# Kernel optimization log

Hardware: AMD Instinct MI355X
Metric: run time of the kernel (lower is better)

The kernel has to match this reference:

```python
import math
import jax, jax.numpy as jnp
import numpy as np

B, N, D, Pd, L, H = 2, 384, 256, 64, 8, 8
Dh = D // H
VOCAB = 21


def _layernorm(x, w, b, eps=1e-5):
    m = jnp.mean(x, axis=-1, keepdims=True)
    v = jnp.var(x, axis=-1, keepdims=True)
    return (x - m) * jax.lax.rsqrt(v + eps) * w + b


def _safe_norm(v):
    return jnp.sqrt(jnp.sum(v * v, axis=-1, keepdims=True) + 1e-8)


def _rot6d(r6):
    # Zhou et al. 6D rotation -> 3x3 via Gram-Schmidt (rows b1,b2,b3)
    a1, a2 = r6[..., :3], r6[..., 3:6]
    b1 = a1 / _safe_norm(a1)
    a2p = a2 - jnp.sum(b1 * a2, axis=-1, keepdims=True) * b1
    b2 = a2p / _safe_norm(a2p)
    b3 = jnp.cross(b1, b2)
    return jnp.stack([b1, b2, b3], axis=-2)  # [..., 3, 3]


def _pos_enc(n, d):
    pos = jnp.arange(n, dtype=jnp.float32)[:, None]
    div = jnp.exp(jnp.arange(0, d, 2, dtype=jnp.float32) * (-math.log(10000.0) / d))
    ang = pos * div  # [n, d/2]
    return jnp.zeros((n, d), jnp.float32).at[:, 0::2].set(jnp.sin(ang)).at[:, 1::2].set(jnp.cos(ang))


def _se3_frame_attention(Q, K, V, frames):
    # Frame-conditioned attention: dot-product scores biased by squared
    # distance between frame translations (IPA-style point bias).
    t = frames[..., :3, 3]                                   # [B,N,3]
    d2 = jnp.sum((t[:, :, None] - t[:, None, :]) ** 2, -1)   # [B,N,N]
    s = jnp.einsum('bihd,bjhd->bhij', Q, K) / math.sqrt(Dh) - d2[:, None]
    a = jax.nn.softmax(s, axis=-1)
    return jnp.einsum('bhij,bjhd->bihd', a, V)               # [B,N,H,Dh]


def _encode(tokens, tok_emb, emb_ln_w, emb_ln_b, Wq, Wk, Wv, Wo, bo,
            attn_ln_w, attn_ln_b, ff_ln_w, ff_ln_b, W1, b1, W2, b2,
            Wop, bop, relpos_emb, pair_ln_w, pair_ln_b, Wf1, bf1, Wf2, bf2):
    Bb, Nn = tokens.shape
    x = tok_emb[tokens] + _pos_enc(Nn, D)[None]
    x = _layernorm(x, emb_ln_w, emb_ln_b)
    frames = jnp.broadcast_to(jnp.eye(4, dtype=x.dtype), (Bb, Nn, 4, 4))
    pos = jnp.arange(Nn)
    rel = jnp.clip(pos[None, :] - pos[:, None], -64, 64) + 64  # rel[i,j]=pos[j]-pos[i]
    rel_e = relpos_emb[rel]                                    # [N,N,Pd]
    bot = jnp.broadcast_to(jnp.array([0.0, 0.0, 0.0, 1.0], x.dtype), (Bb, Nn, 1, 4))
    for l in range(L):
        # SE3 attention block (dropout = identity in eval)
        Q = (x @ Wq[l]).reshape(Bb, Nn, H, Dh)
        Kh = (x @ Wk[l]).reshape(Bb, Nn, H, Dh)
        Vh = (x @ Wv[l]).reshape(Bb, Nn, H, Dh)
        ao = _se3_frame_attention(Q, Kh, Vh, frames).reshape(Bb, Nn, D)
        x = _layernorm(x + ao @ Wo[l] + bo[l], attn_ln_w[l], attn_ln_b[l])
        # FFN (pre-LN inside the Sequential), residual add
        h = _layernorm(x, ff_ln_w[l], ff_ln_b[l])
        x = x + (jax.nn.gelu(h @ W1[l] + b1[l], approximate=False) @ W2[l] + b2[l])
        # Pair features
        proj = jax.nn.relu(x @ Wop + bop)                      # [B,N,Pd]
        pair = _layernorm(proj[:, :, None] + proj[:, None, :] + rel_e[None],
                          pair_ln_w, pair_ln_b)                # [B,N,N,Pd]
        # Frame head
        feat = jnp.concatenate([x, pair.mean(axis=2)], axis=-1)
        raw = jax.nn.silu(feat @ Wf1 + bf1) @ Wf2 + bf2        # [B,N,9]
        R = _rot6d(raw[..., :6])
        trans = raw[..., 6:]
        top = jnp.concatenate([R, trans[..., None]], axis=-1)  # [B,N,3,4]
        frames = jnp.concatenate([top, bot], axis=-2)          # [B,N,4,4]
    return frames, x


def setup_inputs() -> dict:
    key = jax.random.key(0)
    ks = iter(jax.random.split(key, 16))
    def w(shape, scale):
        return (jax.random.normal(next(ks), shape) * scale).astype(jnp.float32)
    return {
        'tokens': jax.random.randint(next(ks), (B, N), 0, VOCAB, dtype=jnp.int32),
        'tok_emb': w((VOCAB, D), 0.02),
        'emb_ln_w': jnp.ones((D,), jnp.float32), 'emb_ln_b': jnp.zeros((D,), jnp.float32),
        'Wq': w((L, D, D), D ** -0.5), 'Wk': w((L, D, D), D ** -0.5),
        'Wv': w((L, D, D), D ** -0.5), 'Wo': w((L, D, D), D ** -0.5),
        'bo': jnp.zeros((L, D), jnp.float32),
        'attn_ln_w': jnp.ones((L, D), jnp.float32), 'attn_ln_b': jnp.zeros((L, D), jnp.float32),
        'ff_ln_w': jnp.ones((L, D), jnp.float32), 'ff_ln_b': jnp.zeros((L, D), jnp.float32),
        'W1': w((L, D, 4 * D), D ** -0.5), 'b1': jnp.zeros((L, 4 * D), jnp.float32),
        'W2': w((L, 4 * D, D), (4 * D) ** -0.5), 'b2': jnp.zeros((L, D), jnp.float32),
        'Wop': w((D, Pd), D ** -0.5), 'bop': jnp.zeros((Pd,), jnp.float32),
        'relpos_emb': w((129, Pd), 0.02),
        'pair_ln_w': jnp.ones((Pd,), jnp.float32), 'pair_ln_b': jnp.zeros((Pd,), jnp.float32),
        'Wf1': w((D + Pd, 128), (D + Pd) ** -0.5), 'bf1': jnp.zeros((128,), jnp.float32),
        'Wf2': w((128, 9), 128 ** -0.5), 'bf2': jnp.zeros((9,), jnp.float32),
    }


def reference(tokens, tok_emb, emb_ln_w, emb_ln_b, Wq, Wk, Wv, Wo, bo,
              attn_ln_w, attn_ln_b, ff_ln_w, ff_ln_b, W1, b1, W2, b2,
              Wop, bop, relpos_emb, pair_ln_w, pair_ln_b, Wf1, bf1, Wf2, bf2):
    return _encode(tokens, tok_emb, emb_ln_w, emb_ln_b, Wq, Wk, Wv, Wo, bo,
                   attn_ln_w, attn_ln_b, ff_ln_w, ff_ln_b, W1, b1, W2, b2,
                   Wop, bop, relpos_emb, pair_ln_w, pair_ln_b, Wf1, bf1, Wf2, bf2)
```

## Files before the change

### kernel.cpp

```cpp
#include <hip/hip_runtime.h>
#include <hip/hip_bf16.h>
#include <math.h>

#define B_  2
#define N_  384
#define D_  256
#define PD_ 64
#define L_  8
#define H_  8
#define DH_ 32
#define GR  4
#define IT  8
#define RT_ 132

__global__ void prologue_kernel(const int* __restrict__ tokens, const float* __restrict__ tok_emb,
                                const float* __restrict__ lnw, const float* __restrict__ lnb,
                                const float* __restrict__ relpos,
                                float* __restrict__ x, float* __restrict__ frames,
                                float* __restrict__ tx, float* __restrict__ ty,
                                float* __restrict__ tz,
                                float* __restrict__ relc, float* __restrict__ relcT) {
  int row = blockIdx.x;
  int n = row % N_;
  int d = threadIdx.x;
  __shared__ float rbuf[256];
  __shared__ float smr;
  if (d < 16) frames[row * 16 + d] = (d == 0 || d == 5 || d == 10 || d == 15) ? 1.0f : 0.0f;
  if (d == 16) tx[row] = 0.0f;
  if (d == 17) ty[row] = 0.0f;
  if (d == 18) tz[row] = 0.0f;
  if (row < 129 && d >= 192) {
    int lane = d & 63;
    float s = relpos[row * PD_ + lane];
    #pragma unroll
    for (int off = 32; off >= 1; off >>= 1) s += __shfl_xor(s, off, 64);
    if (lane == 0) smr = s * (1.0f / PD_);
  }
  int tok = tokens[row];
  float val = tok_emb[tok * D_ + d];
  int i = d >> 1;
  float dv = expf((float)(2 * i) * (-logf(10000.0f) / (float)D_));
  float ang = (float)n * dv;
  val += (d & 1) ? cosf(ang) : sinf(ang);
  rbuf[d] = val; __syncthreads();
  for (int s = 128; s > 0; s >>= 1) { if (d < s) rbuf[d] += rbuf[d + s]; __syncthreads(); }
  float mean = rbuf[0] / D_;
  __syncthreads();
  rbuf[d] = val * val; __syncthreads();
  for (int s = 128; s > 0; s >>= 1) { if (d < s) rbuf[d] += rbuf[d + s]; __syncthreads(); }
  float var = rbuf[0] / D_ - mean * mean;
  float r = rsqrtf(var + 1e-5f);
  x[row * D_ + d] = (val - mean) * r * lnw[d] + lnb[d];
  if (row < 129 && d < PD_) {
    float cv = relpos[row * PD_ + d] - smr;
    relc[row * PD_ + d] = cv;
    relcT[d * RT_ + row] = cv;
  }
}

__device__ __forceinline__ void qkv_unit(int bid, int tid, const float* __restrict__ x,
                                         const float* __restrict__ Wq, const float* __restrict__ Wk,
                                         const float* __restrict__ Wv,
                                         float* __restrict__ q, float* __restrict__ kt,
                                         float* __restrict__ v, float* sA) {
  int tile = bid & 3;
  int m = (bid >> 2) % 3;
  int r0 = (bid / 12) * GR;
  float* red = sA + GR * D_;
  {
    int r = tid >> 6, lane = tid & 63;
    ((float4*)(sA + r * D_))[lane] = ((const float4*)(x + (size_t)(r0 + r) * D_))[lane];
  }
  __syncthreads();
  const float* W = (m == 0) ? Wq : (m == 1) ? Wk : Wv;
  int kc = tid >> 6, c = tid & 63;
  const float* wp = W + (size_t)(kc * 64) * D_ + tile * 64 + c;
  const float* s0 = sA + kc * 64;
  float a0 = 0.f, a1 = 0.f, a2 = 0.f, a3 = 0.f;
  for (int kk = 0; kk < 64; kk += 4) {
    float w0 = wp[(size_t)kk * D_], w1 = wp[(size_t)(kk + 1) * D_];
    float w2 = wp[(size_t)(kk + 2) * D_], w3 = wp[(size_t)(kk + 3) * D_];
    float4 h0 = *(const float4*)(s0 + 0 * D_ + kk);
    float4 h1 = *(const float4*)(s0 + 1 * D_ + kk);
    float4 h2 = *(const float4*)(s0 + 2 * D_ + kk);
    float4 h3 = *(const float4*)(s0 + 3 * D_ + kk);
    a0 = fmaf(h0.x, w0, fmaf(h0.y, w1, fmaf(h0.z, w2, fmaf(h0.w, w3, a0))));
    a1 = fmaf(h1.x, w0, fmaf(h1.y, w1, fmaf(h1.z, w2, fmaf(h1.w, w3, a1))));
    a2 = fmaf(h2.x, w0, fmaf(h2.y, w1, fmaf(h2.z, w2, fmaf(h2.w, w3, a2))));
    a3 = fmaf(h3.x, w0, fmaf(h3.y, w1, fmaf(h3.z, w2, fmaf(h3.w, w3, a3))));
  }
  red[(kc * 4 + 0) * 64 + c] = a0;
  red[(kc * 4 + 1) * 64 + c] = a1;
  red[(kc * 4 + 2) * 64 + c] = a2;
  red[(kc * 4 + 3) * 64 + c] = a3;
  __syncthreads();
  int r = tid >> 6;
  float s = red[(0 * 4 + r) * 64 + c] + red[(1 * 4 + r) * 64 + c]
          + red[(2 * 4 + r) * 64 + c] + red[(3 * 4 + r) * 64 + c];
  int col = tile * 64 + c;
  int row = r0 + r;
  if (m == 1) {
    int b = row / N_, j = row % N_;
    int hh = col >> 5, dd = col & 31;
    kt[((size_t)(b * H_ + hh) * DH_ + dd) * N_ + j] = s;
  } else {
    float* O = (m == 0) ? q : v;
    O[(size_t)row * D_ + col] = s;
  }
}

__device__ __forceinline__ void proj_unit(int row, int tid, const float* __restrict__ x,
                                          const float* __restrict__ Wop, const float* __restrict__ bop,
                                          float* __restrict__ projc, float* __restrict__ projcT,
                                          float* smem) {
  float* sA  = smem;
  float* red = smem + 256;
  if (tid < 64) ((float4*)sA)[tid] = ((const float4*)(x + (size_t)row * D_))[tid];
  __syncthreads();
  int kc = tid >> 6, c = tid & 63;
  const float* wp = Wop + (kc * 64) * PD_ + c;
  const float* s0 = sA + kc * 64;
  float a0 = 0.f, a1 = 0.f, a2 = 0.f, a3 = 0.f;
  for (int kk = 0; kk < 64; kk += 4) {
    a0 = fmaf(s0[kk],     wp[(kk)     * PD_], a0);
    a1 = fmaf(s0[kk + 1], wp[(kk + 1) * PD_], a1);
    a2 = fmaf(s0[kk + 2], wp[(kk + 2) * PD_], a2);
    a3 = fmaf(s0[kk + 3], wp[(kk + 3) * PD_], a3);
  }
  red[kc * 64 + c] = (a0 + a1) + (a2 + a3);
  __syncthreads();
  if (tid < 64) {
    float acc = fmaxf(bop[tid] + red[tid] + red[64 + tid] + red[128 + tid] + red[192 + tid], 0.0f);
    float s = acc;
    #pragma unroll
    for (int off = 32; off >= 1; off >>= 1) s += __shfl_xor(s, off, 64);
    float cv = acc - s * (1.0f / PD_);
    projc[row * PD_ + tid] = cv;
    projcT[(size_t)tid * (B_ * N_) + row] = cv;
  }
}

__global__ void qkv_kernel(const float* __restrict__ x, const float* __restrict__ Wq,
                           const float* __restrict__ Wk, const float* __restrict__ Wv,
                           float* __restrict__ q, float* __restrict__ kt, float* __restrict__ v) {
  __shared__ __align__(16) float smem[2048];
  qkv_unit(blockIdx.x, threadIdx.x, x, Wq, Wk, Wv, q, kt, v, smem);
}

__global__ void proj_qkv_kernel(const float* __restrict__ x,
                                const float* __restrict__ Wop, const float* __restrict__ bop,
                                float* __restrict__ projc, float* __restrict__ projcT,
                                const float* __restrict__ Wq, const float* __restrict__ Wk,
                                const float* __restrict__ Wv,
                                float* __restrict__ q, float* __restrict__ kt,
                                float* __restrict__ v) {
  __shared__ __align__(16) float smem[2048];
  int bid = blockIdx.x, tid = threadIdx.x;
  if (bid < B_ * N_) proj_unit(bid, tid, x, Wop, bop, projc, projcT, smem);
  else               qkv_unit(bid - B_ * N_, tid, x, Wq, Wk, Wv, q, kt, v, smem);
}

__global__ void wo_ln_kernel(const float* __restrict__ ao, const float* __restrict__ Wo,
                             const float* __restrict__ bo,
                             const float* __restrict__ lnw, const float* __restrict__ lnb,
                             float* __restrict__ x) {
  int r0 = blockIdx.x * 2;
  int tid = threadIdx.x;
  int wave = tid >> 6, lane = tid & 63;
  __shared__ __align__(16) float sAO[2 * D_];
  __shared__ float wred[4][4];
  if (tid < 128) ((float4*)sAO)[tid] = ((const float4*)(ao + (size_t)r0 * D_))[tid];
  __syncthreads();
  const float* wp = Wo + tid;
  float a0 = 0.f, a1 = 0.f, a2 = 0.f, a3 = 0.f;
  float c0 = 0.f, c1 = 0.f, c2 = 0.f, c3 = 0.f;
  for (int kk = 0; kk < D_; kk += 4) {
    float w0 = wp[(size_t)kk * D_], w1 = wp[(size_t)(kk + 1) * D_];
    float w2 = wp[(size_t)(kk + 2) * D_], w3 = wp[(size_t)(kk + 3) * D_];
    float4 h0 = *(const float4*)(sAO + kk);
    float4 h1 = *(const float4*)(sAO + D_ + kk);
    a0 = fmaf(h0.x, w0, a0); a1 = fmaf(h0.y, w1, a1);
    a2 = fmaf(h0.z, w2, a2); a3 = fmaf(h0.w, w3, a3);
    c0 = fmaf(h1.x, w0, c0); c1 = fmaf(h1.y, w1, c1);
    c2 = fmaf(h1.z, w2, c2); c3 = fmaf(h1.w, w3, c3);
  }
  float bb = bo[tid];
  float v0 = x[(size_t)r0 * D_ + tid]       + bb + (a0 + a1) + (a2 + a3);
  float v1 = x[(size_t)(r0 + 1) * D_ + tid] + bb + (c0 + c1) + (c2 + c3);
  float s0 = v0, q0 = v0 * v0, s1 = v1, q1 = v1 * v1;
  #pragma unroll
  for (int off = 32; off >= 1; off >>= 1) {
    s0 += __shfl_xor(s0, off, 64); q0 += __shfl_xor(q0, off, 64);
    s1 += __shfl_xor(s1, off, 64); q1 += __shfl_xor(q1, off, 64);
  }
  if (lane == 0) {
    wred[0][wave] = s0; wred[1][wave] = q0;
    wred[2][wave] = s1; wred[3][wave] = q1;
  }
  __syncthreads();
  float S0 = wred[0][0] + wred[0][1] + wred[0][2] + wred[0][3];
  float Q0 = wred[1][0] + wred[1][1] + wred[1][2] + wred[1][3];
  float S1 = wred[2][0] + wred[2][1] + wred[2][2] + wred[2][3];
  float Q1 = wred[3][0] + wred[3][1] + wred[3][2] + wred[3][3];
  float m0 = S0 * (1.0f / D_), m1 = S1 * (1.0f / D_);
  float r0v = rsqrtf(Q0 * (1.0f / D_) - m0 * m0 + 1e-5f);
  float r1v = rsqrtf(Q1 * (1.0f / D_) - m1 * m1 + 1e-5f);
  float wv = lnw[tid], bv = lnb[tid];
  x[(size_t)r0 * D_ + tid]       = (v0 - m0) * r0v * wv + bv;
  x[(size_t)(r0 + 1) * D_ + tid] = (v1 - m1) * r1v * wv + bv;
}

__global__ void gemm4t_kernel(const float* __restrict__ A, const float* __restrict__ W,
                              const float* __restrict__ bias, const float* __restrict__ resid,
                              float* __restrict__ C, int K, int Nc) {
  int tiles = Nc >> 5;
  int bid = blockIdx.x;
  int tile = bid % tiles;
  int r0 = (bid / tiles) * GR;
  int tid = threadIdx.x;
  extern __shared__ __align__(16) float sA[];
  float* red = sA + GR * K;
  {
    int r = tid >> 6, lane = tid & 63;
    for (int kk = lane; kk < (K >> 2); kk += 64)
      ((float4*)(sA + r * K))[kk] = ((const float4*)(A + (size_t)(r0 + r) * K))[kk];
  }
  __syncthreads();
  int kc = tid >> 5, c = tid & 31;
  int KC = K >> 3;
  const float* wp = W + (size_t)(kc * KC) * Nc + tile * 32 + c;
  const float* s0 = sA + kc * KC;
  float a0 = 0.f, a1 = 0.f, a2 = 0.f, a3 = 0.f;
  for (int kk = 0; kk < KC; kk += 4) {
    float w0 = wp[(size_t)kk * Nc], w1 = wp[(size_t)(kk + 1) * Nc];
    float w2 = wp[(size_t)(kk + 2) * Nc], w3 = wp[(size_t)(kk + 3) * Nc];
    float4 h0 = *(const float4*)(s0 + 0 * K + kk);
    float4 h1 = *(const float4*)(s0 + 1 * K + kk);
    float4 h2 = *(const float4*)(s0 + 2 * K + kk);
    float4 h3 = *(const float4*)(s0 + 3 * K + kk);
    a0 = fmaf(h0.x, w0, fmaf(h0.y, w1, fmaf(h0.z, w2, fmaf(h0.w, w3, a0))));
    a1 = fmaf(h1.x, w0, fmaf(h1.y, w1, fmaf(h1.z, w2, fmaf(h1.w, w3, a1))));
    a2 = fmaf(h2.x, w0, fmaf(h2.y, w1, fmaf(h2.z, w2, fmaf(h2.w, w3, a2))));
    a3 = fmaf(h3.x, w0, fmaf(h3.y, w1, fmaf(h3.z, w2, fmaf(h3.w, w3, a3))));
  }
  red[(kc * 4 + 0) * 32 + c] = a0;
  red[(kc * 4 + 1) * 32 + c] = a1;
  red[(kc * 4 + 2) * 32 + c] = a2;
  red[(kc * 4 + 3) * 32 + c] = a3;
  __syncthreads();
  if (tid < GR * 32) {
    int r = tid >> 5, cc = tid & 31;
    float s = 0.f;
    #pragma unroll
    for (int k8 = 0; k8 < 8; k8++) s += red[(k8 * 4 + r) * 32 + cc];
    int col = tile * 32 + cc;
    if (bias)  s += bias[col];
    if (resid) s += resid[(size_t)(r0 + r) * Nc + col];
    C[(size_t)(r0 + r) * Nc + col] = s;
  }
}

__global__ void ff1_kernel(const float* __restrict__ x,
                           const float* __restrict__ lnw, const float* __restrict__ lnb,
                           const float* __restrict__ W1, const float* __restrict__ b1,
                           float* __restrict__ f) {
  int bid = blockIdx.x;
  int tile = bid & 7;
  int r0 = (bid >> 3) * GR;
  int tid = threadIdx.x;
  __shared__ __align__(16) float sA[GR * D_];
  __shared__ float red[2 * GR * 128];
  {
    int r = tid >> 6, lane = tid & 63;
    float4 v = ((const float4*)(x + (size_t)(r0 + r) * D_))[lane];
    float s = v.x + v.y + v.z + v.w;
    float s2 = v.x * v.x + v.y * v.y + v.z * v.z + v.w * v.w;
    #pragma unroll
    for (int off = 32; off >= 1; off >>= 1) {
      s  += __shfl_xor(s, off, 64);
      s2 += __shfl_xor(s2, off, 64);
    }
    float mean = s * (1.0f / D_);
    float var = s2 * (1.0f / D_) - mean * mean;
    float rin = rsqrtf(var + 1e-5f);
    float4 w4 = ((const float4*)lnw)[lane];
    float4 b4 = ((const float4*)lnb)[lane];
    float4 nv;
    nv.x = (v.x - mean) * rin * w4.x + b4.x;
    nv.y = (v.y - mean) * rin * w4.y + b4.y;
    nv.z = (v.z - mean) * rin * w4.z + b4.z;
    nv.w = (v.w - mean) * rin * w4.w + b4.w;
    ((float4*)(sA + r * D_))[lane] = nv;
  }
  __syncthreads();
  int kc = tid >> 7, c = tid & 127;
  int col = tile * 128 + c;
  const float* wp = W1 + (size_t)(kc * 128) * 1024 + col;
  const float* s0 = sA + kc * 128;
  float a0 = 0.f, a1 = 0.f, a2 = 0.f, a3 = 0.f;
  for (int kk = 0; kk < 128; kk += 4) {
    float w0 = wp[(size_t)kk * 1024], w1 = wp[(size_t)(kk + 1) * 1024];
    float w2 = wp[(size_t)(kk + 2) * 1024], w3 = wp[(size_t)(kk + 3) * 1024];
    float4 h0 = *(const float4*)(s0 + 0 * D_ + kk);
    float4 h1 = *(const float4*)(s0 + 1 * D_ + kk);
    float4 h2 = *(const float4*)(s0 + 2 * D_ + kk);
    float4 h3 = *(const float4*)(s0 + 3 * D_ + kk);
    a0 = fmaf(h0.x, w0, fmaf(h0.y, w1, fmaf(h0.z, w2, fmaf(h0.w, w3, a0))));
    a1 = fmaf(h1.x, w0, fmaf(h1.y, w1, fmaf(h1.z, w2, fmaf(h1.w, w3, a1))));
    a2 = fmaf(h2.x, w0, fmaf(h2.y, w1, fmaf(h2.z, w2, fmaf(h2.w, w3, a2))));
    a3 = fmaf(h3.x, w0, fmaf(h3.y, w1, fmaf(h3.z, w2, fmaf(h3.w, w3, a3))));
  }
  red[(kc * 4 + 0) * 128 + c] = a0;
  red[(kc * 4 + 1) * 128 + c] = a1;
  red[(kc * 4 + 2) * 128 + c] = a2;
  red[(kc * 4 + 3) * 128 + c] = a3;
  __syncthreads();
  int rA = tid >> 7;
  #pragma unroll
  for (int p = 0; p < 2; p++) {
    int r = rA + p * 2;
    float s = red[(0 * 4 + r) * 128 + c] + red[(1 * 4 + r) * 128 + c] + b1[col];
    s = 0.5f * s * (1.0f + erff(s * 0.7071067811865475f));
    f[(size_t)(r0 + r) * 1024 + col] = s;
  }
}

__global__ void attn_kernel(const float* __restrict__ Q, const float* __restrict__ KT,
                            const float* __restrict__ V,
                            const float* __restrict__ tx, const float* __restrict__ ty,
                            const float* __restrict__ tz, float* __restrict__ AO) {
  const int TILES = N_ / IT;
  int bid = blockIdx.x;
  int it = bid % TILES;
  int h  = (bid / TILES) % H_;
  int b  = bid / (TILES * H_);
  int i0 = it * IT;
  int tid = threadIdx.x;
  int wave = tid >> 6, lane = tid & 63;

  __shared__ __align__(16) float sQ[IT * DH_];
  __shared__ __align__(16) float sK[DH_ * 64];
  __shared__ __align__(16) float sV[64 * DH_];
  __shared__ __align__(16) float sS[IT][N_];
  __shared__ float sti[3][IT];
  __shared__ float sinv[IT];

  {
    int ii = tid >> 5, d = tid & 31;
    sQ[ii * DH_ + d] = Q[((size_t)(b * N_ + i0 + ii)) * D_ + h * DH_ + d];
  }
  if (tid < IT) {
    sti[0][tid] = tx[b * N_ + i0 + tid];
    sti[1][tid] = ty[b * N_ + i0 + tid];
    sti[2][tid] = tz[b * N_ + i0 + tid];
  }
  const float* ktb = KT + (size_t)(b * H_ + h) * DH_ * N_;
  const float* vb  = V + (size_t)b * N_ * D_ + h * DH_;
  const float* txb = tx + b * N_;
  const float* tyb = ty + b * N_;
  const float* tzb = tz + b * N_;
  __syncthreads();

  float4 q0r[8], q1r[8];
  #pragma unroll
  for (int t = 0; t < 8; t++) {
    q0r[t] = ((const float4*)(sQ + (wave * 2 + 0) * DH_))[t];
    q1r[t] = ((const float4*)(sQ + (wave * 2 + 1) * DH_))[t];
  }

  for (int jc = 0; jc < N_; jc += 64) {
    for (int idx = tid; idx < DH_ * 64; idx += 256) {
      int d = idx >> 6, jj = idx & 63;
      sK[d * 64 + jj] = ktb[(size_t)d * N_ + jc + jj];
    }
    __syncthreads();
    int jj = lane;
    float tjx = txb[jc + jj], tjy = tyb[jc + jj], tjz = tzb[jc + jj];
    float a0 = 0.f, a1 = 0.f;
    #pragma unroll
    for (int t = 0; t < 8; t++) {
      float k0 = sK[(4 * t + 0) * 64 + jj];
      float k1 = sK[(4 * t + 1) * 64 + jj];
      float k2 = sK[(4 * t + 2) * 64 + jj];
      float k3 = sK[(4 * t + 3) * 64 + jj];
      float4 qa = q0r[t], qb = q1r[t];
      a0 = fmaf(qa.x, k0, fmaf(qa.y, k1, fmaf(qa.z, k2, fmaf(qa.w, k3, a0))));
      a1 = fmaf(qb.x, k0, fmaf(qb.y, k1, fmaf(qb.z, k2, fmaf(qb.w, k3, a1))));
    }
    #pragma unroll
    for (int s = 0; s < 2; s++) {
      int ii = wave * 2 + s;
      float a = (s == 0) ? a0 : a1;
      float dx = sti[0][ii] - tjx;
      float dy = sti[1][ii] - tjy;
      float dz = sti[2][ii] - tjz;
      sS[ii][jc + jj] = a * 0.17677669529663689f - (dx * dx + dy * dy + dz * dz);
    }
    __syncthreads();
  }

  #pragma unroll
  for (int s = 0; s < 2; s++) {
    int ii = wave * 2 + s;
    float vrow[6];
    float m = -1e30f;
    #pragma unroll
    for (int t = 0; t < 6; t++) { vrow[t] = sS[ii][t * 64 + lane]; m = fmaxf(m, vrow[t]); }
    #pragma unroll
    for (int off = 32; off >= 1; off >>= 1) m = fmaxf(m, __shfl_xor(m, off, 64));
    float ps = 0.f;
    #pragma unroll
    for (int t = 0; t < 6; t++) {
      float e = expf(vrow[t] - m);
      sS[ii][t * 64 + lane] = e;
      ps += e;
    }
    #pragma unroll
    for (int off = 32; off >= 1; off >>= 1) ps += __shfl_xor(ps, off, 64);
    if (lane == 0) sinv[ii] = 1.0f / ps;
  }
  __syncthreads();

  int ii = tid >> 5, dd = tid & 31;
  float o0 = 0.f, o1 = 0.f;
  for (int jc = 0; jc < N_; jc += 64) {
    for (int idx = tid; idx < 64 * DH_; idx += 256) {
      int jj = idx >> 5, d = idx & 31;
      sV[jj * DH_ + d] = vb[(size_t)(jc + jj) * D_ + d];
    }
    __syncthreads();
    const float* srow = &sS[ii][jc];
    #pragma unroll
    for (int jj = 0; jj < 64; jj += 4) {
      float4 sv = *(const float4*)(srow + jj);
      o0 = fmaf(sv.x, sV[(jj + 0) * DH_ + dd], o0);
      o1 = fmaf(sv.y, sV[(jj + 1) * DH_ + dd], o1);
      o0 = fmaf(sv.z, sV[(jj + 2) * DH_ + dd], o0);
      o1 = fmaf(sv.w, sV[(jj + 3) * DH_ + dd], o1);
    }
    __syncthreads();
  }
  AO[((size_t)(b * N_ + i0 + ii)) * D_ + h * DH_ + dd] = (o0 + o1) * sinv[ii];
}

__global__ void pair_head_kernel(const float* __restrict__ projc, const float* __restrict__ projcT,
                                 const float* __restrict__ relc, const float* __restrict__ relcT,
                                 const float* __restrict__ lnw, const float* __restrict__ lnb,
                                 const float* __restrict__ x,
                                 const float* __restrict__ Wf1, const float* __restrict__ bWf1,
                                 const float* __restrict__ Wf2, const float* __restrict__ bWf2,
                                 float* __restrict__ frames, float* __restrict__ tx,
                                 float* __restrict__ ty, float* __restrict__ tz) {
  const int M = B_ * N_;
  int row = blockIdx.x;
  int b = row / N_;
  int i = row % N_;
  int tid = threadIdx.x;
  int lane = tid & 63;
  int wave = tid >> 6;
  __shared__ float svpi[PD_];
  __shared__ float sr[N_];
  __shared__ float red[4][PD_];
  __shared__ float sfeat[320];
  __shared__ float fred[2][128];
  __shared__ float sg[128];
  __shared__ float sraw[9];

  if (tid < PD_) svpi[tid] = projc[row * PD_ + tid];
  if (tid < D_) sfeat[tid] = x[(size_t)row * D_ + tid];
  __syncthreads();

  {
    int jA = tid;
    int raA = jA - i; raA = raA < -64 ? -64 : (raA > 64 ? 64 : raA); raA += 64;
    const float* pA = projcT + b * N_ + jA;
    const float* rA = relcT + raA;
    float s2A = 0.f;
    #pragma unroll 8
    for (int c = 0; c < PD_; c++) {
      float dA = svpi[c] + pA[(size_t)c * M] + rA[c * RT_];
      s2A = fmaf(dA, dA, s2A);
    }
    sr[jA] = rsqrtf(s2A * (1.0f / PD_) + 1e-5f);
    if (tid < 128) {
      int jB = tid + 256;
      int raB = jB - i; raB = raB < -64 ? -64 : (raB > 64 ? 64 : raB); raB += 64;
      const float* pB = projcT + b * N_ + jB;
      const float* rB = relcT + raB;
      float s2B = 0.f;
      #pragma unroll 8
      for (int c = 0; c < PD_; c++) {
        float dB = svpi[c] + pB[(size_t)c * M] + rB[c * RT_];
        s2B = fmaf(dB, dB, s2B);
      }
      sr[jB] = rsqrtf(s2B * (1.0f / PD_) + 1e-5f);
    }
  }
  __syncthreads();

  {
    float vpl = svpi[lane];
    const float* pb = projc + (size_t)b * N_ * PD_;
    float acc = 0.0f;
    for (int j = wave * 2; j < N_; j += 8) {
      int ja = j, jb = j + 1;
      int ra = ja - i; ra = ra < -64 ? -64 : (ra > 64 ? 64 : ra); ra += 64;
      int rb = jb - i; rb = rb < -64 ? -64 : (rb > 64 ? 64 : rb); rb += 64;
      float da = vpl + pb[ja * PD_ + lane] + relc[ra * PD_ + lane];
      float db = vpl + pb[jb * PD_ + lane] + relc[rb * PD_ + lane];
      acc = fmaf(da, sr[ja], fmaf(db, sr[jb], acc));
    }
    red[wave][lane] = acc;
  }
  __syncthreads();
  if (wave == 0) {
    float s = red[0][lane] + red[1][lane] + red[2][lane] + red[3][lane];
    sfeat[D_ + lane] = lnb[lane] + s * lnw[lane] * (1.0f / N_);
  }
  __syncthreads();

  int kc = tid >> 7, c = tid & 127;
  int koff = kc * 160;
  const float* wp = Wf1 + (size_t)koff * 128 + c;
  const float* s0 = sfeat + koff;
  float a0 = 0.f, a1 = 0.f, a2 = 0.f, a3 = 0.f;
  for (int kk = 0; kk < 160; kk += 4) {
    a0 = fmaf(s0[kk],     wp[(size_t)kk * 128],       a0);
    a1 = fmaf(s0[kk + 1], wp[(size_t)(kk + 1) * 128], a1);
    a2 = fmaf(s0[kk + 2], wp[(size_t)(kk + 2) * 128], a2);
    a3 = fmaf(s0[kk + 3], wp[(size_t)(kk + 3) * 128], a3);
  }
  fred[kc][c] = (a0 + a1) + (a2 + a3);
  __syncthreads();
  if (tid < 128) {
    float g = fred[0][tid] + fred[1][tid] + bWf1[tid];
    sg[tid] = g / (1.0f + expf(-g));
  }
  __syncthreads();

  if (tid < 9) {
    float b0 = 0.f, b1v = 0.f;
    for (int kk = 0; kk < 128; kk += 2) {
      b0  = fmaf(sg[kk],     Wf2[(kk)     * 9 + tid], b0);
      b1v = fmaf(sg[kk + 1], Wf2[(kk + 1) * 9 + tid], b1v);
    }
    sraw[tid] = bWf2[tid] + b0 + b1v;
  }
  __syncthreads();
  if (tid == 0) {
    float a1x = sraw[0], a1y = sraw[1], a1z = sraw[2];
    float a2x = sraw[3], a2y = sraw[4], a2z = sraw[5];
    float n1 = sqrtf(a1x * a1x + a1y * a1y + a1z * a1z + 1e-8f);
    float b1x = a1x / n1, b1y = a1y / n1, b1z = a1z / n1;
    float dp = b1x * a2x + b1y * a2y + b1z * a2z;
    float px = a2x - dp * b1x, py = a2y - dp * b1y, pz = a2z - dp * b1z;
    float n2 = sqrtf(px * px + py * py + pz * pz + 1e-8f);
    float b2x = px / n2, b2y = py / n2, b2z = pz / n2;
    float b3x = b1y * b2z - b1z * b2y;
    float b3y = b1z * b2x - b1x * b2z;
    float b3z = b1x * b2y - b1y * b2x;
    float* f = frames + row * 16;
    f[0]  = b1x; f[1]  = b1y; f[2]  = b1z; f[3]  = sraw[6];
    f[4]  = b2x; f[5]  = b2y; f[6]  = b2z; f[7]  = sraw[7];
    f[8]  = b3x; f[9]  = b3y; f[10] = b3z; f[11] = sraw[8];
    f[12] = 0.0f; f[13] = 0.0f; f[14] = 0.0f; f[15] = 1.0f;
    tx[row] = sraw[6];
    ty[row] = sraw[7];
    tz[row] = sraw[8];
  }
}

__global__ void write_out_kernel(const float* __restrict__ frames, const float* __restrict__ x,
                                 float* __restrict__ out) {
  int i = blockIdx.x * 256 + threadIdx.x;
  const int nf = B_ * N_ * 16;
  const int total = nf + B_ * N_ * D_;
  if (i < nf) out[i] = frames[i];
  else if (i < total) out[i] = x[i - nf];
}

extern "C" void kernel_launch(void* const* d_in, const int* in_sizes, int n_in,
                              void* d_out, int out_size, void* d_ws, size_t ws_size,
                              hipStream_t stream) {
  const int*   tokens    = (const int*)  d_in[0];
  const float* tok_emb   = (const float*)d_in[1];
  const float* emb_ln_w  = (const float*)d_in[2];
  const float* emb_ln_b  = (const float*)d_in[3];
  const float* Wq        = (const float*)d_in[4];
  const float* Wk        = (const float*)d_in[5];
  const float* Wv        = (const float*)d_in[6];
  const float* Wo        = (const float*)d_in[7];
  const float* bo        = (const float*)d_in[8];
  const float* attn_ln_w = (const float*)d_in[9];
  const float* attn_ln_b = (const float*)d_in[10];
  const float* ff_ln_w   = (const float*)d_in[11];
  const float* ff_ln_b   = (const float*)d_in[12];
  const float* W1        = (const float*)d_in[13];
  const float* b1        = (const float*)d_in[14];
  const float* W2        = (const float*)d_in[15];
  const float* b2        = (const float*)d_in[16];
  const float* Wop       = (const float*)d_in[17];
  const float* bop       = (const float*)d_in[18];
  const float* relpos    = (const float*)d_in[19];
  const float* pair_ln_w = (const float*)d_in[20];
  const float* pair_ln_b = (const float*)d_in[21];
  const float* Wf1       = (const float*)d_in[22];
  const float* bWf1      = (const float*)d_in[23];
  const float* Wf2       = (const float*)d_in[24];
  const float* bWf2      = (const float*)d_in[25];

  const int M = B_ * N_;
  const int XE = M * D_;
  float* ws     = (float*)d_ws;
  float* frames = ws;
  float* projc  = frames + M * 16;
  float* projcT = projc  + M * PD_;
  float* relc   = projcT + M * PD_;
  float* relcT  = relc   + 8320;
  float* tx     = relcT  + 8448;
  float* ty     = tx     + M;
  float* tz     = ty     + M;
  float* x      = tz     + M;
  float* q      = x  + XE;
  float* kt     = q  + XE;
  float* v      = kt + XE;
  float* ao     = v  + XE;
  float* f      = q;

  prologue_kernel<<<M, 256, 0, stream>>>(tokens, tok_emb, emb_ln_w, emb_ln_b, relpos,
                                         x, frames, tx, ty, tz, relc, relcT);
  qkv_kernel<<<(M / GR) * 12, 256, 0, stream>>>(x, Wq, Wk, Wv, q, kt, v);

  const size_t lds_ff2 = (GR * 1024 + 1024) * sizeof(float);

  for (int l = 0; l < L_; l++) {
    attn_kernel<<<B_ * H_ * (N_ / IT), 256, 0, stream>>>(q, kt, v, tx, ty, tz, ao);
    wo_ln_kernel<<<M / 2, 256, 0, stream>>>(ao, Wo + (size_t)l * D_ * D_, bo + l * D_,
                                            attn_ln_w + l * D_, attn_ln_b + l * D_, x);
    ff1_kernel<<<(M / GR) * 8, 256, 0, stream>>>(x, ff_ln_w + l * D_, ff_ln_b + l * D_,
                                                 W1 + (size_t)l * D_ * 1024, b1 + l * 1024, f);
    gemm4t_kernel<<<(M / GR) * 8, 256, lds_ff2, stream>>>(
        f, W2 + (size_t)l * 1024 * D_, b2 + l * D_, x, x, 1024, D_);
    if (l < L_ - 1) {
      int lq = l + 1;
      proj_qkv_kernel<<<M + (M / GR) * 12, 256, 0, stream>>>(
          x, Wop, bop, projc, projcT,
          Wq + (size_t)lq * D_ * D_, Wk + (size_t)lq * D_ * D_, Wv + (size_t)lq * D_ * D_,
          q, kt, v);
    } else {
      proj_qkv_kernel<<<M, 256, 0, stream>>>(x, Wop, bop, projc, projcT, Wq, Wk, Wv, q, kt, v);
    }
    pair_head_kernel<<<M, 256, 0, stream>>>(projc, projcT, relc, relcT, pair_ln_w, pair_ln_b,
                                            x, Wf1, bWf1, Wf2, bWf2, frames, tx, ty, tz);
  }

  const int total = B_ * N_ * 16 + B_ * N_ * D_;
  write_out_kernel<<<(total + 255) / 256, 256, 0, stream>>>(frames, x, (float*)d_out);
}
```

Before: 1.005 ms.

## Fuse FF1 and FF2 into one kernel with atomic split-K accumulation

Merges the W1+GELU kernel and the W2 GEMM into one kernel. Each block computes a 128-wide slice of the hidden activation, keeps it in shared memory, and multiplies it by the matching W2 rows. Partial outputs are summed into a residual buffer that wo_ln zeroes beforehand, using atomicAdd, and tile 0 adds the bias and residual. This removes one launch and the round trip of the 1024-wide intermediate through global memory, at the cost of float atomics and nondeterministic summation order.

```diff
diff --git a/kernel.cpp b/kernel.cpp
--- a/kernel.cpp
+++ b/kernel.cpp
@@ -163,7 +163,7 @@
 __global__ void wo_ln_kernel(const float* __restrict__ ao, const float* __restrict__ Wo,
                              const float* __restrict__ bo,
                              const float* __restrict__ lnw, const float* __restrict__ lnb,
-                             float* __restrict__ x) {
+                             float* xio, float* __restrict__ xout) {
   int r0 = blockIdx.x * 2;
   int tid = threadIdx.x;
   int wave = tid >> 6, lane = tid & 63;
@@ -185,8 +185,8 @@
     c2 = fmaf(h1.z, w2, c2); c3 = fmaf(h1.w, w3, c3);
   }
   float bb = bo[tid];
-  float v0 = x[(size_t)r0 * D_ + tid]       + bb + (a0 + a1) + (a2 + a3);
-  float v1 = x[(size_t)(r0 + 1) * D_ + tid] + bb + (c0 + c1) + (c2 + c3);
+  float v0 = xio[(size_t)r0 * D_ + tid]       + bb + (a0 + a1) + (a2 + a3);
+  float v1 = xio[(size_t)(r0 + 1) * D_ + tid] + bb + (c0 + c1) + (c2 + c3);
   float s0 = v0, q0 = v0 * v0, s1 = v1, q1 = v1 * v1;
   #pragma unroll
   for (int off = 32; off >= 1; off >>= 1) {
@@ -206,73 +206,27 @@
   float r0v = rsqrtf(Q0 * (1.0f / D_) - m0 * m0 + 1e-5f);
   float r1v = rsqrtf(Q1 * (1.0f / D_) - m1 * m1 + 1e-5f);
   float wv = lnw[tid], bv = lnb[tid];
-  x[(size_t)r0 * D_ + tid]       = (v0 - m0) * r0v * wv + bv;
-  x[(size_t)(r0 + 1) * D_ + tid] = (v1 - m1) * r1v * wv + bv;
-}
-
-__global__ void gemm4t_kernel(const float* __restrict__ A, const float* __restrict__ W,
-                              const float* __restrict__ bias, const float* __restrict__ resid,
-                              float* __restrict__ C, int K, int Nc) {
-  int tiles = Nc >> 5;
-  int bid = blockIdx.x;
-  int tile = bid % tiles;
-  int r0 = (bid / tiles) * GR;
-  int tid = threadIdx.x;
-  extern __shared__ __align__(16) float sA[];
-  float* red = sA + GR * K;
-  {
-    int r = tid >> 6, lane = tid & 63;
-    for (int kk = lane; kk < (K >> 2); kk += 64)
-      ((float4*)(sA + r * K))[kk] = ((const float4*)(A + (size_t)(r0 + r) * K))[kk];
-  }
-  __syncthreads();
-  int kc = tid >> 5, c = tid & 31;
-  int KC = K >> 3;
-  const float* wp = W + (size_t)(kc * KC) * Nc + tile * 32 + c;
-  const float* s0 = sA + kc * KC;
-  float a0 = 0.f, a1 = 0.f, a2 = 0.f, a3 = 0.f;
-  for (int kk = 0; kk < KC; kk += 4) {
-    float w0 = wp[(size_t)kk * Nc], w1 = wp[(size_t)(kk + 1) * Nc];
-    float w2 = wp[(size_t)(kk + 2) * Nc], w3 = wp[(size_t)(kk + 3) * Nc];
-    float4 h0 = *(const float4*)(s0 + 0 * K + kk);
-    float4 h1 = *(const float4*)(s0 + 1 * K + kk);
-    float4 h2 = *(const float4*)(s0 + 2 * K + kk);
-    float4 h3 = *(const float4*)(s0 + 3 * K + kk);
-    a0 = fmaf(h0.x, w0, fmaf(h0.y, w1, fmaf(h0.z, w2, fmaf(h0.w, w3, a0))));
-    a1 = fmaf(h1.x, w0, fmaf(h1.y, w1, fmaf(h1.z, w2, fmaf(h1.w, w3, a1))));
-    a2 = fmaf(h2.x, w0, fmaf(h2.y, w1, fmaf(h2.z, w2, fmaf(h2.w, w3, a2))));
-    a3 = fmaf(h3.x, w0, fmaf(h3.y, w1, fmaf(h3.z, w2, fmaf(h3.w, w3, a3))));
-  }
-  red[(kc * 4 + 0) * 32 + c] = a0;
-  red[(kc * 4 + 1) * 32 + c] = a1;
-  red[(kc * 4 + 2) * 32 + c] = a2;
-  red[(kc * 4 + 3) * 32 + c] = a3;
-  __syncthreads();
-  if (tid < GR * 32) {
-    int r = tid >> 5, cc = tid & 31;
-    float s = 0.f;
-    #pragma unroll
-    for (int k8 = 0; k8 < 8; k8++) s += red[(k8 * 4 + r) * 32 + cc];
-    int col = tile * 32 + cc;
-    if (bias)  s += bias[col];
-    if (resid) s += resid[(size_t)(r0 + r) * Nc + col];
-    C[(size_t)(r0 + r) * Nc + col] = s;
-  }
-}
-
-__global__ void ff1_kernel(const float* __restrict__ x,
-                           const float* __restrict__ lnw, const float* __restrict__ lnb,
-                           const float* __restrict__ W1, const float* __restrict__ b1,
-                           float* __restrict__ f) {
+  xout[(size_t)r0 * D_ + tid]       = (v0 - m0) * r0v * wv + bv;
+  xout[(size_t)(r0 + 1) * D_ + tid] = (v1 - m1) * r1v * wv + bv;
+  xio[(size_t)r0 * D_ + tid]       = 0.0f;
+  xio[(size_t)(r0 + 1) * D_ + tid] = 0.0f;
+}
+
+__global__ void ff_fused_kernel(const float* __restrict__ xs,
+                                const float* __restrict__ lnw, const float* __restrict__ lnb,
+                                const float* __restrict__ W1, const float* __restrict__ b1,
+                                const float* __restrict__ W2, const float* __restrict__ b2v,
+                                float* __restrict__ xacc) {
   int bid = blockIdx.x;
   int tile = bid & 7;
   int r0 = (bid >> 3) * GR;
   int tid = threadIdx.x;
   __shared__ __align__(16) float sA[GR * D_];
   __shared__ float red[2 * GR * 128];
+  __shared__ __align__(16) float sF[128 * 4];
   {
     int r = tid >> 6, lane = tid & 63;
-    float4 v = ((const float4*)(x + (size_t)(r0 + r) * D_))[lane];
+    float4 v = ((const float4*)(xs + (size_t)(r0 + r) * D_))[lane];
     float s = v.x + v.y + v.z + v.w;
     float s2 = v.x * v.x + v.y * v.y + v.z * v.z + v.w * v.w;
     #pragma unroll
@@ -293,35 +247,63 @@
     ((float4*)(sA + r * D_))[lane] = nv;
   }
   __syncthreads();
-  int kc = tid >> 7, c = tid & 127;
-  int col = tile * 128 + c;
-  const float* wp = W1 + (size_t)(kc * 128) * 1024 + col;
-  const float* s0 = sA + kc * 128;
-  float a0 = 0.f, a1 = 0.f, a2 = 0.f, a3 = 0.f;
-  for (int kk = 0; kk < 128; kk += 4) {
-    float w0 = wp[(size_t)kk * 1024], w1 = wp[(size_t)(kk + 1) * 1024];
-    float w2 = wp[(size_t)(kk + 2) * 1024], w3 = wp[(size_t)(kk + 3) * 1024];
-    float4 h0 = *(const float4*)(s0 + 0 * D_ + kk);
-    float4 h1 = *(const float4*)(s0 + 1 * D_ + kk);
-    float4 h2 = *(const float4*)(s0 + 2 * D_ + kk);
-    float4 h3 = *(const float4*)(s0 + 3 * D_ + kk);
-    a0 = fmaf(h0.x, w0, fmaf(h0.y, w1, fmaf(h0.z, w2, fmaf(h0.w, w3, a0))));
-    a1 = fmaf(h1.x, w0, fmaf(h1.y, w1, fmaf(h1.z, w2, fmaf(h1.w, w3, a1))));
-    a2 = fmaf(h2.x, w0, fmaf(h2.y, w1, fmaf(h2.z, w2, fmaf(h2.w, w3, a2))));
-    a3 = fmaf(h3.x, w0, fmaf(h3.y, w1, fmaf(h3.z, w2, fmaf(h3.w, w3, a3))));
-  }
-  red[(kc * 4 + 0) * 128 + c] = a0;
-  red[(kc * 4 + 1) * 128 + c] = a1;
-  red[(kc * 4 + 2) * 128 + c] = a2;
-  red[(kc * 4 + 3) * 128 + c] = a3;
-  __syncthreads();
-  int rA = tid >> 7;
-  #pragma unroll
-  for (int p = 0; p < 2; p++) {
-    int r = rA + p * 2;
-    float s = red[(0 * 4 + r) * 128 + c] + red[(1 * 4 + r) * 128 + c] + b1[col];
-    s = 0.5f * s * (1.0f + erff(s * 0.7071067811865475f));
-    f[(size_t)(r0 + r) * 1024 + col] = s;
+  {
+    int kc = tid >> 7, c = tid & 127;
+    int col = tile * 128 + c;
+    const float* wp = W1 + (size_t)(kc * 128) * 1024 + col;
+    const float* s0 = sA + kc * 128;
+    float a0 = 0.f, a1 = 0.f, a2 = 0.f, a3 = 0.f;
+    for (int kk = 0; kk < 128; kk += 4) {
+      float w0 = wp[(size_t)kk * 1024], w1 = wp[(size_t)(kk + 1) * 1024];
+      float w2 = wp[(size_t)(kk + 2) * 1024], w3 = wp[(size_t)(kk + 3) * 1024];
+      float4 h0 = *(const float4*)(s0 + 0 * D_ + kk);
+      float4 h1 = *(const float4*)(s0 + 1 * D_ + kk);
+      float4 h2 = *(const float4*)(s0 + 2 * D_ + kk);
+      float4 h3 = *(const float4*)(s0 + 3 * D_ + kk);
+      a0 = fmaf(h0.x, w0, fmaf(h0.y, w1, fmaf(h0.z, w2, fmaf(h0.w, w3, a0))));
+      a1 = fmaf(h1.x, w0, fmaf(h1.y, w1, fmaf(h1.z, w2, fmaf(h1.w, w3, a1))));
+      a2 = fmaf(h2.x, w0, fmaf(h2.y, w1, fmaf(h2.z, w2, fmaf(h2.w, w3, a2))));
+      a3 = fmaf(h3.x, w0, fmaf(h3.y, w1, fmaf(h3.z, w2, fmaf(h3.w, w3, a3))));
+    }
+    red[(kc * 4 + 0) * 128 + c] = a0;
+    red[(kc * 4 + 1) * 128 + c] = a1;
+    red[(kc * 4 + 2) * 128 + c] = a2;
+    red[(kc * 4 + 3) * 128 + c] = a3;
+  }
+  __syncthreads();
+  {
+    int rA = tid >> 7, c = tid & 127;
+    int col = tile * 128 + c;
+    #pragma unroll
+    for (int p = 0; p < 2; p++) {
+      int r = rA + p * 2;
+      float s = red[(0 * 4 + r) * 128 + c] + red[(1 * 4 + r) * 128 + c] + b1[col];
+      s = 0.5f * s * (1.0f + erff(s * 0.7071067811865475f));
+      sF[c * 4 + r] = s;
+    }
+  }
+  __syncthreads();
+  {
+    const float* w2p = W2 + (size_t)(tile * 128) * D_ + tid;
+    float o0 = 0.f, o1 = 0.f, o2 = 0.f, o3 = 0.f;
+    #pragma unroll 8
+    for (int k = 0; k < 128; k++) {
+      float w = w2p[(size_t)k * D_];
+      float4 f4 = *(const float4*)(sF + k * 4);
+      o0 = fmaf(f4.x, w, o0); o1 = fmaf(f4.y, w, o1);
+      o2 = fmaf(f4.z, w, o2); o3 = fmaf(f4.w, w, o3);
+    }
+    if (tile == 0) {
+      float bb2 = b2v[tid];
+      o0 += xs[(size_t)(r0 + 0) * D_ + tid] + bb2;
+      o1 += xs[(size_t)(r0 + 1) * D_ + tid] + bb2;
+      o2 += xs[(size_t)(r0 + 2) * D_ + tid] + bb2;
+      o3 += xs[(size_t)(r0 + 3) * D_ + tid] + bb2;
+    }
+    atomicAdd(&xacc[(size_t)(r0 + 0) * D_ + tid], o0);
+    atomicAdd(&xacc[(size_t)(r0 + 1) * D_ + tid], o1);
+    atomicAdd(&xacc[(size_t)(r0 + 2) * D_ + tid], o2);
+    atomicAdd(&xacc[(size_t)(r0 + 3) * D_ + tid], o3);
   }
 }
 
@@ -620,40 +602,38 @@
   float* tx     = relcT  + 8448;
   float* ty     = tx     + M;
   float* tz     = ty     + M;
-  float* x      = tz     + M;
-  float* q      = x  + XE;
+  float* xb     = tz     + M;
+  float* q      = xb + XE;
   float* kt     = q  + XE;
   float* v      = kt + XE;
   float* ao     = v  + XE;
-  float* f      = q;
+  float* xa     = ao + XE;
 
   prologue_kernel<<<M, 256, 0, stream>>>(tokens, tok_emb, emb_ln_w, emb_ln_b, relpos,
-                                         x, frames, tx, ty, tz, relc, relcT);
-  qkv_kernel<<<(M / GR) * 12, 256, 0, stream>>>(x, Wq, Wk, Wv, q, kt, v);
-
-  const size_t lds_ff2 = (GR * 1024 + 1024) * sizeof(float);
+                                         xb, frames, tx, ty, tz, relc, relcT);
+  qkv_kernel<<<(M / GR) * 12, 256, 0, stream>>>(xb, Wq, Wk, Wv, q, kt, v);
 
   for (int l = 0; l < L_; l++) {
     attn_kernel<<<B_ * H_ * (N_ / IT), 256, 0, stream>>>(q, kt, v, tx, ty, tz, ao);
     wo_ln_kernel<<<M / 2, 256, 0, stream>>>(ao, Wo + (size_t)l * D_ * D_, bo + l * D_,
-                                            attn_ln_w + l * D_, attn_ln_b + l * D_, x);
-    ff1_kernel<<<(M / GR) * 8, 256, 0, stream>>>(x, ff_ln_w + l * D_, ff_ln_b + l * D_,
-                                                 W1 + (size_t)l * D_ * 1024, b1 + l * 1024, f);
-    gemm4t_kernel<<<(M / GR) * 8, 256, lds_ff2, stream>>>(
-        f, W2 + (size_t)l * 1024 * D_, b2 + l * D_, x, x, 1024, D_);
+                                            attn_ln_w + l * D_, attn_ln_b + l * D_, xb, xa);
+    ff_fused_kernel<<<(M / GR) * 8, 256, 0, stream>>>(
+        xa, ff_ln_w + l * D_, ff_ln_b + l * D_,
+        W1 + (size_t)l * D_ * 1024, b1 + l * 1024,
+        W2 + (size_t)l * 1024 * D_, b2 + l * D_, xb);
     if (l < L_ - 1) {
       int lq = l + 1;
       proj_qkv_kernel<<<M + (M / GR) * 12, 256, 0, stream>>>(
-          x, Wop, bop, projc, projcT,
+          xb, Wop, bop, projc, projcT,
           Wq + (size_t)lq * D_ * D_, Wk + (size_t)lq * D_ * D_, Wv + (size_t)lq * D_ * D_,
           q, kt, v);
     } else {
-      proj_qkv_kernel<<<M, 256, 0, stream>>>(x, Wop, bop, projc, projcT, Wq, Wk, Wv, q, kt, v);
+      proj_qkv_kernel<<<M, 256, 0, stream>>>(xb, Wop, bop, projc, projcT, Wq, Wk, Wv, q, kt, v);
     }
     pair_head_kernel<<<M, 256, 0, stream>>>(projc, projcT, relc, relcT, pair_ln_w, pair_ln_b,
-                                            x, Wf1, bWf1, Wf2, bWf2, frames, tx, ty, tz);
+                                            xb, Wf1, bWf1, Wf2, bWf2, frames, tx, ty, tz);
   }
 
   const int total = B_ * N_ * 16 + B_ * N_ * D_;
-  write_out_kernel<<<(total + 255) / 256, 256, 0, stream>>>(frames, x, (float*)d_out);
-}
+  write_out_kernel<<<(total + 255) / 256, 256, 0, stream>>>(frames, xb, (float*)d_out);
+}
```

Measured after the change: 920.7 us. 1.09x faster.
